# Kernel optimization log

Measured on AMD Instinct MI355X. Metric: run time of the kernel, lower is better.

## Reference

```python
import jax, jax.numpy as jnp
import numpy as np

B, NPG, DEG, F, H, C = 256, 256, 16, 128, 128, 10
N = B * NPG
E = N * DEG
RATIO = 0.5
K1 = int(np.ceil(RATIO * NPG))       # 128
K2 = int(np.ceil(RATIO * K1))        # 64
K3 = int(np.ceil(RATIO * K2))        # 32


def _glorot(key, shape):
    lim = np.sqrt(6.0 / (shape[0] + shape[1]))
    return jax.random.uniform(key, shape, jnp.float32, -lim, lim)


def setup_inputs() -> dict:
    key = jax.random.key(0)
    ks = jax.random.split(key, 16)
    x = jax.random.normal(ks[0], (N, F), jnp.float32)
    epg = E // B
    g = jnp.repeat(jnp.arange(B, dtype=jnp.int32), epg)
    src = jax.random.randint(ks[1], (E,), 0, NPG, jnp.int32) + g * NPG
    dst = jax.random.randint(ks[2], (E,), 0, NPG, jnp.int32) + g * NPG
    edge_index = jnp.stack([src, dst])
    batch = jnp.repeat(jnp.arange(B, dtype=jnp.int32), NPG)
    return {
        "x": x, "edge_index": edge_index, "batch": batch,
        "W1": _glorot(ks[3], (F, H)), "b1": jnp.zeros((H,), jnp.float32),
        "Wp1": _glorot(ks[4], (H, 1)), "bp1": jnp.zeros((1,), jnp.float32),
        "W2": _glorot(ks[5], (H, H)), "b2": jnp.zeros((H,), jnp.float32),
        "Wp2": _glorot(ks[6], (H, 1)), "bp2": jnp.zeros((1,), jnp.float32),
        "W3": _glorot(ks[7], (H, H)), "b3": jnp.zeros((H,), jnp.float32),
        "Wp3": _glorot(ks[8], (H, 1)), "bp3": jnp.zeros((1,), jnp.float32),
        "Wl1": _glorot(ks[9], (2 * H, H)), "bl1": jnp.zeros((H,), jnp.float32),
        "Wl2": _glorot(ks[10], (H, H // 2)), "bl2": jnp.zeros((H // 2,), jnp.float32),
        "Wl3": _glorot(ks[11], (H // 2, C)), "bl3": jnp.zeros((C,), jnp.float32),
    }


def gcn_conv(x, src, dst, emask, nmask, W, b):
    # PyG GCNConv: symmetric normalization with self-loops, edge weights = emask.
    h = x @ W
    deg = jax.ops.segment_sum(emask, dst, num_segments=N) + nmask  # self-loop on active nodes
    dinv = jnp.where(deg > 0, jax.lax.rsqrt(deg), 0.0)
    w = emask * dinv[src] * dinv[dst]                      # [E]
    agg = jax.ops.segment_sum(h[src] * w[:, None], dst, num_segments=N)
    out = agg + h * (dinv * dinv * nmask)[:, None] + b
    return out * nmask[:, None]


def topk_pool(x, src, dst, emask, nmask, Wp, bp, k):
    # SAGPool-style gcn_pool: score via GCNConv(H->1), per-graph top-k,
    # x <- x * tanh(score) on kept nodes, edges restricted to kept nodes.
    s = gcn_conv(x, src, dst, emask, nmask, Wp, bp)[:, 0]   # [N]
    sm = jnp.where(nmask > 0, s, -jnp.inf).reshape(B, NPG)
    idx = jax.lax.top_k(sm, k)[1]                           # [B,k]
    newmask = jnp.zeros((B, NPG), x.dtype).at[jnp.arange(B)[:, None], idx].set(1.0).reshape(-1)
    x_new = x * jnp.tanh(s)[:, None] * newmask[:, None]
    emask_new = emask * newmask[src] * newmask[dst]
    return x_new, emask_new, newmask


def readout(x, nmask, batch):
    # cat([global_max_pool, global_mean_pool]) over remaining nodes per graph
    cnt = jax.ops.segment_sum(nmask, batch, num_segments=B)
    mean = jax.ops.segment_sum(x, batch, num_segments=B) / cnt[:, None]
    xinf = jnp.where(nmask[:, None] > 0, x, -jnp.inf)
    mx = jax.ops.segment_max(xinf, batch, num_segments=B)
    return jnp.concatenate([mx, mean], axis=1)


def reference(x, edge_index, batch, W1, b1, Wp1, bp1, W2, b2, Wp2, bp2, W3, b3, Wp3, bp3,
              Wl1, bl1, Wl2, bl2, Wl3, bl3):
    src, dst = edge_index[0], edge_index[1]
    emask = jnp.ones((E,), x.dtype)
    nmask = jnp.ones((N,), x.dtype)

    h = jax.nn.relu(gcn_conv(x, src, dst, emask, nmask, W1, b1))
    h, emask, nmask = topk_pool(h, src, dst, emask, nmask, Wp1, bp1, K1)
    x1 = readout(h, nmask, batch)

    h = jax.nn.relu(gcn_conv(h, src, dst, emask, nmask, W2, b2))
    h, emask, nmask = topk_pool(h, src, dst, emask, nmask, Wp2, bp2, K2)
    x2 = readout(h, nmask, batch)

    h = jax.nn.relu(gcn_conv(h, src, dst, emask, nmask, W3, b3))
    h, emask, nmask = topk_pool(h, src, dst, emask, nmask, Wp3, bp3, K3)
    x3 = readout(h, nmask, batch)

    z = x1 + x2 + x3
    z = jax.nn.relu(z @ Wl1 + bl1)   # dropout is identity in eval mode
    z = jax.nn.relu(z @ Wl2 + bl2)
    return jax.nn.log_softmax(z @ Wl3 + bl3, axis=-1)
```

## Files before the change

kernel.cpp:

```cpp
#include <hip/hip_runtime.h>
#include <math.h>

#define NB   256
#define NPG  256
#define NN   (NB * NPG)
#define NE   (NN * 16)
#define EPG  (NE / NB)
#define FD   128
#define NC   10
#define NSL  32
#define NEG_INF (-3.402823466e38f)

struct SM {
    float hs[NPG][FD];
    int   rp[NPG + 4];
    float dvv[NPG];
    float sw[NPG];
    float sf[NPG];
    float svv[NPG];
    float th[NPG];
    float zacc[2 * FD];
    int   si[NPG];
    int   kept[NPG];
    int   anode[NPG];
    int   wsum[16];
    float red_mx[16][FD];
    float red_sm[16][FD];
    unsigned char colb[EPG];
};

__device__ __forceinline__ float4& hsq(SM& sm, int v, int q) {
    return *(float4*)&sm.hs[v][(q ^ (v & 7)) << 2];
}

template <int NACT, bool LAST>
__device__ __forceinline__ void do_level(SM& sm,
                                         const float* __restrict__ Wmat,
                                         const float* __restrict__ bias,
                                         const float* __restrict__ Wp,
                                         const float* __restrict__ bpp,
                                         int tid) {
    constexpr int NPS = NACT / NSL;
    constexpr int K   = NACT / 2;
    constexpr int TPN = 1024 / NACT;
    const int f4 = tid & 31;
    const int s  = tid >> 5;

    {
        int vr[NPS];
        float4 acc[NPS];
#pragma unroll
        for (int c = 0; c < NPS; ++c) {
            vr[c] = sm.anode[c * NSL + s];
            acc[c] = make_float4(0.f, 0.f, 0.f, 0.f);
        }
#pragma unroll 2
        for (int kq = 0; kq < 32; ++kq) {
            const int k0 = kq << 2;
            float4 w0 = *(const float4*)&Wmat[(k0 + 0) * FD + 4 * f4];
            float4 w1 = *(const float4*)&Wmat[(k0 + 1) * FD + 4 * f4];
            float4 w2 = *(const float4*)&Wmat[(k0 + 2) * FD + 4 * f4];
            float4 w3 = *(const float4*)&Wmat[(k0 + 3) * FD + 4 * f4];
#pragma unroll
            for (int c = 0; c < NPS; ++c) {
                float4 hv = hsq(sm, vr[c], kq);
                acc[c].x += hv.x * w0.x + hv.y * w1.x + hv.z * w2.x + hv.w * w3.x;
                acc[c].y += hv.x * w0.y + hv.y * w1.y + hv.z * w2.y + hv.w * w3.y;
                acc[c].z += hv.x * w0.z + hv.y * w1.z + hv.z * w2.z + hv.w * w3.z;
                acc[c].w += hv.x * w0.w + hv.y * w1.w + hv.z * w2.w + hv.w * w3.w;
            }
        }
#pragma unroll
        for (int c = 0; c < NPS; ++c) {
            const float d = sm.dvv[vr[c]];
            acc[c].x *= d; acc[c].y *= d; acc[c].z *= d; acc[c].w *= d;
            hsq(sm, vr[c], f4) = acc[c];
        }
    }
    __syncthreads();

    const float4 b4  = *(const float4*)&bias[4 * f4];
    const float4 wp4 = *(const float4*)&Wp[4 * f4];
    float4 hreg[NPS];
#pragma unroll
    for (int c = 0; c < NPS; ++c) {
        const int v = sm.anode[c * NSL + s];
        const float dv_ = sm.dvv[v];
        float4 S = hsq(sm, v, f4);
        const int e0 = sm.rp[v], e1 = sm.rp[v + 1];
        int e = e0;
        int ea = (e0 + 3) & ~3;
        if (ea > e1) ea = e1;
        for (; e < ea; ++e) {
            float4 hu = hsq(sm, sm.colb[e], f4);
            S.x += hu.x; S.y += hu.y; S.z += hu.z; S.w += hu.w;
        }
        for (; e + 4 <= e1; e += 4) {
            unsigned p = *(const unsigned*)&sm.colb[e];
            int u0 = p & 255, u1 = (p >> 8) & 255;
            int u2 = (p >> 16) & 255, u3 = p >> 24;
            float4 h0 = hsq(sm, u0, f4);
            float4 h1 = hsq(sm, u1, f4);
            float4 h2 = hsq(sm, u2, f4);
            float4 h3 = hsq(sm, u3, f4);
            S.x += h0.x + h1.x + h2.x + h3.x;
            S.y += h0.y + h1.y + h2.y + h3.y;
            S.z += h0.z + h1.z + h2.z + h3.z;
            S.w += h0.w + h1.w + h2.w + h3.w;
        }
        for (; e < e1; ++e) {
            float4 hu = hsq(sm, sm.colb[e], f4);
            S.x += hu.x; S.y += hu.y; S.z += hu.z; S.w += hu.w;
        }
        float4 acc;
        acc.x = fmaxf(S.x * dv_ + b4.x, 0.f);
        acc.y = fmaxf(S.y * dv_ + b4.y, 0.f);
        acc.z = fmaxf(S.z * dv_ + b4.z, 0.f);
        acc.w = fmaxf(S.w * dv_ + b4.w, 0.f);
        hreg[c] = acc;
        float p = acc.x * wp4.x + acc.y * wp4.y + acc.z * wp4.z + acc.w * wp4.w;
        p += __shfl_xor(p, 1);
        p += __shfl_xor(p, 2);
        p += __shfl_xor(p, 4);
        p += __shfl_xor(p, 8);
        p += __shfl_xor(p, 16);
        if (f4 == 0) sm.sw[v] = p;
    }
    __syncthreads();

    {
        const int i = tid / TPN, sub = tid % TPN;
        const int v = sm.anode[i];
        const float dv_ = sm.dvv[v];
        float part = 0.f;
        const int e1 = sm.rp[v + 1];
        for (int e = sm.rp[v] + sub; e < e1; e += TPN) {
            int u = sm.colb[e];
            part += sm.dvv[u] * sm.sw[u];
        }
#pragma unroll
        for (int o = 1; o < TPN; o <<= 1) part += __shfl_xor(part, o);
        if (sub == 0) {
            float acc = sm.sw[v] * dv_ * dv_ + bpp[0] + dv_ * part;
            sm.sf[v] = acc;
            sm.svv[i] = acc;
        }
    }
    __syncthreads();

    float v_ = 0.f;
    int   id_ = 0;
    if (tid < NACT) { v_ = sm.svv[tid]; id_ = sm.anode[tid]; }
#pragma unroll
    for (int k = 2; k <= NACT; k <<= 1) {
#pragma unroll
        for (int j = k >> 1; j > 0; j >>= 1) {
            if (j < 64) {
                if (tid < NACT) {
                    float vp = __shfl_xor(v_, j);
                    int  idp = __shfl_xor(id_, j);
                    bool up    = ((tid & k) == 0);
                    bool lower = ((tid & j) == 0);
                    bool g = (v_ > vp) || (v_ == vp && id_ < idp);
                    if (g != (lower == up)) { v_ = vp; id_ = idp; }
                }
            } else {
                if (tid < NACT) { sm.svv[tid] = v_; sm.si[tid] = id_; }
                __syncthreads();
                if (tid < NACT) {
                    int p = tid ^ j;
                    float vp = sm.svv[p];
                    int  idp = sm.si[p];
                    bool up    = ((tid & k) == 0);
                    bool lower = ((tid & j) == 0);
                    bool g = (v_ > vp) || (v_ == vp && id_ < idp);
                    if (g != (lower == up)) { v_ = vp; id_ = idp; }
                }
                __syncthreads();
            }
        }
    }
    if (tid < NPG) sm.kept[tid] = 0;
    __syncthreads();
    if (tid < K) {
        sm.kept[id_] = 1;
        sm.th[id_] = tanhf(sm.sf[id_]);
    }
    __syncthreads();

    float4 mx4 = make_float4(NEG_INF, NEG_INF, NEG_INF, NEG_INF);
    float4 sm4 = make_float4(0.f, 0.f, 0.f, 0.f);
#pragma unroll
    for (int c = 0; c < NPS; ++c) {
        const int v = sm.anode[c * NSL + s];
        const int kp = sm.kept[v];
        const float tg = kp ? sm.th[v] : 0.f;
        float4 val;
        val.x = hreg[c].x * tg;
        val.y = hreg[c].y * tg;
        val.z = hreg[c].z * tg;
        val.w = hreg[c].w * tg;
        hsq(sm, v, f4) = val;
        if (kp) {
            mx4.x = fmaxf(mx4.x, val.x);
            mx4.y = fmaxf(mx4.y, val.y);
            mx4.z = fmaxf(mx4.z, val.z);
            mx4.w = fmaxf(mx4.w, val.w);
        }
        sm4.x += val.x; sm4.y += val.y; sm4.z += val.z; sm4.w += val.w;
    }
    mx4.x = fmaxf(mx4.x, __shfl_xor(mx4.x, 32)); sm4.x += __shfl_xor(sm4.x, 32);
    mx4.y = fmaxf(mx4.y, __shfl_xor(mx4.y, 32)); sm4.y += __shfl_xor(sm4.y, 32);
    mx4.z = fmaxf(mx4.z, __shfl_xor(mx4.z, 32)); sm4.z += __shfl_xor(sm4.z, 32);
    mx4.w = fmaxf(mx4.w, __shfl_xor(mx4.w, 32)); sm4.w += __shfl_xor(sm4.w, 32);
    const int wv = tid >> 6;
    if ((tid & 63) < 32) {
        *(float4*)&sm.red_mx[wv][4 * f4] = mx4;
        *(float4*)&sm.red_sm[wv][4 * f4] = sm4;
    }
    if (!LAST) {
        const int n = tid >> 2, sub = tid & 3;
        int cnti = 0;
        const int kpn = sm.kept[n];
        if (kpn) {
            const int e1 = sm.rp[n + 1];
            for (int e = sm.rp[n] + sub; e < e1; e += 4)
                cnti += sm.kept[sm.colb[e]];
        }
        cnti += __shfl_xor(cnti, 1);
        cnti += __shfl_xor(cnti, 2);
        if (sub == 0) sm.dvv[n] = kpn ? rsqrtf(1.f + (float)cnti) : 0.f;
    }
    __syncthreads();
    if (tid < FD) {
        float mx = NEG_INF, smv = 0.f;
#pragma unroll
        for (int i = 0; i < 16; ++i) {
            mx = fmaxf(mx, sm.red_mx[i][tid]);
            smv += sm.red_sm[i][tid];
        }
        sm.zacc[tid] += mx;
        sm.zacc[FD + tid] += smv / (float)K;
    }
    if (tid < K) sm.anode[tid] = id_;
    __syncthreads();
}

__global__ __launch_bounds__(1024)
void k_mega(const float* __restrict__ x, const int* __restrict__ ei,
            const float* __restrict__ W1, const float* __restrict__ b1,
            const float* __restrict__ Wp1, const float* __restrict__ bp1,
            const float* __restrict__ W2, const float* __restrict__ b2,
            const float* __restrict__ Wp2, const float* __restrict__ bp2,
            const float* __restrict__ W3, const float* __restrict__ b3,
            const float* __restrict__ Wp3, const float* __restrict__ bp3,
            const float* __restrict__ Wl1, const float* __restrict__ bl1,
            const float* __restrict__ Wl2, const float* __restrict__ bl2,
            const float* __restrict__ Wl3, const float* __restrict__ bl3,
            float* __restrict__ out) {
    __shared__ SM sm;
    const int g = blockIdx.x, tid = threadIdx.x;
    const int gbase = g * NPG, ebase = g * EPG;
    const int f4 = tid & 31, s = tid >> 5;

    int myd[4], mys[4];
#pragma unroll
    for (int i = 0; i < 4; ++i) {
        int e = ebase + tid + i * 1024;
        myd[i] = ei[NE + e] - gbase;
        mys[i] = ei[e] - gbase;
    }

    if (tid < NPG) sm.si[tid] = 0;
    __syncthreads();
#pragma unroll
    for (int i = 0; i < 4; ++i) atomicAdd(&sm.si[myd[i]], 1);
    __syncthreads();
    int vincl = 0, cnt = 0;
    if (tid < NPG) {
        cnt = sm.si[tid];
        sm.dvv[tid] = rsqrtf(1.f + (float)cnt);
        vincl = cnt;
        const int lane = tid & 63;
#pragma unroll
        for (int o = 1; o < 64; o <<= 1) {
            int n = __shfl_up(vincl, o);
            if (lane >= o) vincl += n;
        }
        if (lane == 63) sm.wsum[tid >> 6] = vincl;
    }
    __syncthreads();
    if (tid < NPG) {
        int base = 0;
        for (int w = 0; w < (tid >> 6); ++w) base += sm.wsum[w];
        int excl = base + vincl - cnt;
        sm.rp[tid] = excl;
        sm.kept[tid] = excl;
        if (tid == 0) sm.rp[NPG] = EPG;
        sm.anode[tid] = tid;
        sm.zacc[tid] = 0.f;
    }
    __syncthreads();
#pragma unroll
    for (int i = 0; i < 4; ++i) {
        int p = atomicAdd(&sm.kept[myd[i]], 1);
        sm.colb[p] = (unsigned char)mys[i];
    }
    for (int r = s; r < NPG; r += NSL)
        hsq(sm, r, f4) =
            *(const float4*)&x[((size_t)(gbase + r)) * FD + 4 * f4];
    __syncthreads();

    do_level<256, false>(sm, W1, b1, Wp1, bp1, tid);
    do_level<128, false>(sm, W2, b2, Wp2, bp2, tid);
    do_level<64,  true >(sm, W3, b3, Wp3, bp3, tid);

    {
        const int o = tid >> 2, sub = tid & 3;
        if (tid < 512) {
            float a = 0.f;
            for (int k = sub; k < 256; k += 4) a += sm.zacc[k] * Wl1[k * 128 + o];
            a += __shfl_xor(a, 1);
            a += __shfl_xor(a, 2);
            if (sub == 0) sm.sw[o] = fmaxf(a + bl1[o], 0.f);
        }
    }
    __syncthreads();
    {
        const int o = tid >> 2, sub = tid & 3;
        if (tid < 256) {
            float a = 0.f;
            for (int k = sub; k < 128; k += 4) a += sm.sw[k] * Wl2[k * 64 + o];
            a += __shfl_xor(a, 1);
            a += __shfl_xor(a, 2);
            if (sub == 0) sm.sf[o] = fmaxf(a + bl2[o], 0.f);
        }
    }
    __syncthreads();
    {
        const int o = tid >> 3, sub = tid & 7;
        if (tid < 8 * NC) {
            float a = 0.f;
            for (int k = sub; k < 64; k += 8) a += sm.sf[k] * Wl3[k * NC + o];
            a += __shfl_xor(a, 1);
            a += __shfl_xor(a, 2);
            a += __shfl_xor(a, 4);
            if (sub == 0) sm.svv[o] = a + bl3[o];
        }
    }
    __syncthreads();
    if (tid == 0) {
        float m = sm.svv[0];
        for (int c = 1; c < NC; ++c) m = fmaxf(m, sm.svv[c]);
        float se = 0.f;
        for (int c = 0; c < NC; ++c) se += expf(sm.svv[c] - m);
        float lse = m + logf(se);
        for (int c = 0; c < NC; ++c) out[g * NC + c] = sm.svv[c] - lse;
    }
}

extern "C" void kernel_launch(void* const* d_in, const int* in_sizes, int n_in,
                              void* d_out, int out_size, void* d_ws, size_t ws_size,
                              hipStream_t stream) {
    const float* x   = (const float*)d_in[0];
    const int*   ei  = (const int*)d_in[1];
    const float* W1  = (const float*)d_in[3];
    const float* b1  = (const float*)d_in[4];
    const float* Wp1 = (const float*)d_in[5];
    const float* bp1 = (const float*)d_in[6];
    const float* W2  = (const float*)d_in[7];
    const float* b2  = (const float*)d_in[8];
    const float* Wp2 = (const float*)d_in[9];
    const float* bp2 = (const float*)d_in[10];
    const float* W3  = (const float*)d_in[11];
    const float* b3  = (const float*)d_in[12];
    const float* Wp3 = (const float*)d_in[13];
    const float* bp3 = (const float*)d_in[14];
    const float* Wl1 = (const float*)d_in[15];
    const float* bl1 = (const float*)d_in[16];
    const float* Wl2 = (const float*)d_in[17];
    const float* bl2 = (const float*)d_in[18];
    const float* Wl3 = (const float*)d_in[19];
    const float* bl3 = (const float*)d_in[20];
    float* out = (float*)d_out;

    k_mega<<<NB, 1024, 0, stream>>>(x, ei,
                                    W1, b1, Wp1, bp1,
                                    W2, b2, Wp2, bp2,
                                    W3, b3, Wp3, bp3,
                                    Wl1, bl1, Wl2, bl2, Wl3, bl3, out);
}
```

Before: 135.1 us.

## Restructure per-level GEMM to row-per-lane with wave-uniform weight columns, prescale inputs by dinv

```diff
diff --git a/kernel.cpp b/kernel.cpp
--- a/kernel.cpp
+++ b/kernel.cpp
@@ -43,39 +43,41 @@
     constexpr int NPS = NACT / NSL;
     constexpr int K   = NACT / 2;
     constexpr int TPN = 1024 / NACT;
+    constexpr int RG  = NACT / 64;
     const int f4 = tid & 31;
     const int s  = tid >> 5;
-
-    {
-        int vr[NPS];
-        float4 acc[NPS];
-#pragma unroll
-        for (int c = 0; c < NPS; ++c) {
-            vr[c] = sm.anode[c * NSL + s];
-            acc[c] = make_float4(0.f, 0.f, 0.f, 0.f);
-        }
+    const int wv_ = tid >> 6, lane = tid & 63;
+
+    float4 a4[8];
+    int myrow = 0, cb = 0;
+    const bool gact = (wv_ < RG * 4);
+    if (gact) {
+        cb = __builtin_amdgcn_readfirstlane(wv_ / RG);
+        myrow = sm.anode[(wv_ % RG) * 64 + lane];
+        const float* __restrict__ Wcb = Wmat + cb * 32;
+#pragma unroll
+        for (int q = 0; q < 8; ++q) a4[q] = make_float4(0.f, 0.f, 0.f, 0.f);
 #pragma unroll 2
         for (int kq = 0; kq < 32; ++kq) {
-            const int k0 = kq << 2;
-            float4 w0 = *(const float4*)&Wmat[(k0 + 0) * FD + 4 * f4];
-            float4 w1 = *(const float4*)&Wmat[(k0 + 1) * FD + 4 * f4];
-            float4 w2 = *(const float4*)&Wmat[(k0 + 2) * FD + 4 * f4];
-            float4 w3 = *(const float4*)&Wmat[(k0 + 3) * FD + 4 * f4];
-#pragma unroll
-            for (int c = 0; c < NPS; ++c) {
-                float4 hv = hsq(sm, vr[c], kq);
-                acc[c].x += hv.x * w0.x + hv.y * w1.x + hv.z * w2.x + hv.w * w3.x;
-                acc[c].y += hv.x * w0.y + hv.y * w1.y + hv.z * w2.y + hv.w * w3.y;
-                acc[c].z += hv.x * w0.z + hv.y * w1.z + hv.z * w2.z + hv.w * w3.z;
-                acc[c].w += hv.x * w0.w + hv.y * w1.w + hv.z * w2.w + hv.w * w3.w;
+            const float4 hv = hsq(sm, myrow, kq);
+#pragma unroll
+            for (int q = 0; q < 8; ++q) {
+                float4 w0 = *(const float4*)&Wcb[(4 * kq + 0) * FD + 4 * q];
+                float4 w1 = *(const float4*)&Wcb[(4 * kq + 1) * FD + 4 * q];
+                float4 w2 = *(const float4*)&Wcb[(4 * kq + 2) * FD + 4 * q];
+                float4 w3 = *(const float4*)&Wcb[(4 * kq + 3) * FD + 4 * q];
+                a4[q].x += hv.x * w0.x + hv.y * w1.x + hv.z * w2.x + hv.w * w3.x;
+                a4[q].y += hv.x * w0.y + hv.y * w1.y + hv.z * w2.y + hv.w * w3.y;
+                a4[q].z += hv.x * w0.z + hv.y * w1.z + hv.z * w2.z + hv.w * w3.z;
+                a4[q].w += hv.x * w0.w + hv.y * w1.w + hv.z * w2.w + hv.w * w3.w;
             }
         }
-#pragma unroll
-        for (int c = 0; c < NPS; ++c) {
-            const float d = sm.dvv[vr[c]];
-            acc[c].x *= d; acc[c].y *= d; acc[c].z *= d; acc[c].w *= d;
-            hsq(sm, vr[c], f4) = acc[c];
-        }
+    }
+    __syncthreads();
+    if (gact) {
+#pragma unroll
+        for (int q = 0; q < 8; ++q)
+            hsq(sm, myrow, cb * 8 + q) = a4[q];
     }
     __syncthreads();
 
@@ -188,6 +190,21 @@
     }
     __syncthreads();
 
+    if (!LAST) {
+        const int n = tid >> 2, sub = tid & 3;
+        int cnti = 0;
+        const int kpn = sm.kept[n];
+        if (kpn) {
+            const int e1 = sm.rp[n + 1];
+            for (int e = sm.rp[n] + sub; e < e1; e += 4)
+                cnti += sm.kept[sm.colb[e]];
+        }
+        cnti += __shfl_xor(cnti, 1);
+        cnti += __shfl_xor(cnti, 2);
+        if (sub == 0) sm.dvv[n] = kpn ? rsqrtf(1.f + (float)cnti) : 0.f;
+        __syncthreads();
+    }
+
     float4 mx4 = make_float4(NEG_INF, NEG_INF, NEG_INF, NEG_INF);
     float4 sm4 = make_float4(0.f, 0.f, 0.f, 0.f);
 #pragma unroll
@@ -200,7 +217,13 @@
         val.y = hreg[c].y * tg;
         val.z = hreg[c].z * tg;
         val.w = hreg[c].w * tg;
-        hsq(sm, v, f4) = val;
+        if (!LAST) {
+            const float dn = sm.dvv[v];
+            float4 st;
+            st.x = val.x * dn; st.y = val.y * dn;
+            st.z = val.z * dn; st.w = val.w * dn;
+            hsq(sm, v, f4) = st;
+        }
         if (kp) {
             mx4.x = fmaxf(mx4.x, val.x);
             mx4.y = fmaxf(mx4.y, val.y);
@@ -213,23 +236,9 @@
     mx4.y = fmaxf(mx4.y, __shfl_xor(mx4.y, 32)); sm4.y += __shfl_xor(sm4.y, 32);
     mx4.z = fmaxf(mx4.z, __shfl_xor(mx4.z, 32)); sm4.z += __shfl_xor(sm4.z, 32);
     mx4.w = fmaxf(mx4.w, __shfl_xor(mx4.w, 32)); sm4.w += __shfl_xor(sm4.w, 32);
-    const int wv = tid >> 6;
     if ((tid & 63) < 32) {
-        *(float4*)&sm.red_mx[wv][4 * f4] = mx4;
-        *(float4*)&sm.red_sm[wv][4 * f4] = sm4;
-    }
-    if (!LAST) {
-        const int n = tid >> 2, sub = tid & 3;
-        int cnti = 0;
-        const int kpn = sm.kept[n];
-        if (kpn) {
-            const int e1 = sm.rp[n + 1];
-            for (int e = sm.rp[n] + sub; e < e1; e += 4)
-                cnti += sm.kept[sm.colb[e]];
-        }
-        cnti += __shfl_xor(cnti, 1);
-        cnti += __shfl_xor(cnti, 2);
-        if (sub == 0) sm.dvv[n] = kpn ? rsqrtf(1.f + (float)cnti) : 0.f;
+        *(float4*)&sm.red_mx[wv_][4 * f4] = mx4;
+        *(float4*)&sm.red_sm[wv_][4 * f4] = sm4;
     }
     __syncthreads();
     if (tid < FD) {
@@ -306,9 +315,12 @@
         int p = atomicAdd(&sm.kept[myd[i]], 1);
         sm.colb[p] = (unsigned char)mys[i];
     }
-    for (int r = s; r < NPG; r += NSL)
-        hsq(sm, r, f4) =
-            *(const float4*)&x[((size_t)(gbase + r)) * FD + 4 * f4];
+    for (int r = s; r < NPG; r += NSL) {
+        const float d = sm.dvv[r];
+        float4 xv = *(const float4*)&x[((size_t)(gbase + r)) * FD + 4 * f4];
+        xv.x *= d; xv.y *= d; xv.z *= d; xv.w *= d;
+        hsq(sm, r, f4) = xv;
+    }
     __syncthreads();
 
     do_level<256, false>(sm, W1, b1, Wp1, bp1, tid);
```

After: 143.9 us. 1.07x slower.
